# Kernel tuning notes

Measured on AMD Instinct MI355X. Metric: run time of the kernel, lower is better.

Reference implementation:

```python
import jax, jax.numpy as jnp
import numpy as np

L_MAX = 3
NR = 3


def _sh_channels(x, y, z):
    # Real spherical harmonic polynomials up to l=3, in the exact channel
    # order produced by the original stack/concat/reshape sequence:
    # [Y00, Y10(z), Y20, Y30,  (Y1_10,Y1_11, Y2_10,Y2_11, Y3_10,Y3_11),
    #  (Y2_20,Y2_21, Y3_20,Y3_21), (Y3_30,Y3_31)]
    pi = np.pi
    x2, y2, z2 = x * x, y * y, z * z
    xy, yz, zx = x * y, y * z, z * x
    x3, y3, z3 = x2 * x, y2 * y, z2 * z
    x2y, y2z, z2x = x2 * y, y2 * z, z2 * x
    x2z, xy2, yz2 = x2 * z, x * y2, y * z2
    xyz = xy * z

    Y00 = jnp.full_like(x, np.sqrt(1.0 / pi) / 2.0)
    c1 = np.sqrt(3.0 / pi) / 2.0
    Y100, Y1_10, Y1_11 = c1 * z, c1 * x, c1 * y
    c2 = np.sqrt(15.0 / pi) / 2.0
    Y200 = np.sqrt(5.0 / pi) / 4.0 * (2.0 * z2 - x2 - y2)
    Y2_10, Y2_11 = c2 * zx, c2 * yz
    Y2_20, Y2_21 = np.sqrt(15.0 / pi) / 4.0 * (x2 - y2), c2 * xy
    c31 = np.sqrt(21.0 / (2.0 * pi)) / 4.0
    Y300 = np.sqrt(7.0 / pi) / 4.0 * (2.0 * z3 - 3.0 * x2z - 3.0 * y2z)
    Y3_10 = c31 * (4.0 * z2x - x3 - xy2)
    Y3_11 = c31 * (4.0 * yz2 - x2y - y3)
    Y3_20 = np.sqrt(105.0 / pi) / 4.0 * (x2z - y2z)
    Y3_21 = np.sqrt(105.0 / pi) / 2.0 * xyz
    c33 = np.sqrt(35.0 / (2.0 * pi)) / 4.0
    Y3_30 = c33 * (x3 - 3.0 * xy2)
    Y3_31 = c33 * (3.0 * x2y - y3)

    return jnp.stack([
        Y00, Y100, Y200, Y300,
        Y1_10, Y1_11, Y2_10, Y2_11, Y3_10, Y3_11,
        Y2_20, Y2_21, Y3_20, Y3_21,
        Y3_30, Y3_31,
    ], axis=-1)  # [..., 16]


def _gaussian_shells(r, n):
    # shell centers evenly spaced in [0, 1]
    centers = jnp.arange(n, dtype=r.dtype) / float(max(n - 1, 1))
    d = r[..., None] - centers  # [..., n]
    g = jnp.exp((4.0 * np.log(0.5)) * (d * d))
    return g / jnp.sum(g, axis=-1, keepdims=True)


def setup_inputs() -> dict:
    key = jax.random.key(0)
    k1, k2, k3 = jax.random.split(key, 3)
    B, V, P = 4, 4096, 64
    patches = jax.random.normal(k1, (B, V, P, 3), dtype=jnp.float32)
    frames = jax.random.normal(k2, (B, V, 3, 3), dtype=jnp.float32)
    r = jax.random.uniform(k3, (B, V, P), dtype=jnp.float32)
    return {"patches": patches, "frames": frames, "r": r}


def reference(patches, frames, r):
    # l2_normalize with tf's eps behavior
    sq = jnp.sum(patches * patches, axis=-1, keepdims=True)
    dirs = patches / jnp.sqrt(jnp.maximum(sq, 1e-12))
    # rotate directions into local frames
    proj = jnp.einsum('bvij,bvpi->bvpj', frames, dirs)  # [B,V,P,3]
    x, y, z = proj[..., 0], proj[..., 1], proj[..., 2]
    Y = _sh_channels(x, y, z)            # [B,V,P,16]
    g = _gaussian_shells(r, NR)          # [B,V,P,NR]
    return g[..., :, None] * Y[..., None, :]  # [B,V,P,NR,16]
```

## Files before the change

kernel.cpp:

```cpp
#include <hip/hip_runtime.h>


#define TPB 256
#define PT_VALS 48
#define SM_STRIDE 49

__global__ __launch_bounds__(TPB) void sph_kernel(
    const float* __restrict__ patches,
    const float* __restrict__ frames,
    const float* __restrict__ rr,
    float* __restrict__ out,
    int n_points)
{
    __shared__ float sm[TPB * SM_STRIDE];
    const int tid = threadIdx.x;
    const int q = blockIdx.x * TPB + tid;

    if (q < n_points) {
        float d0 = patches[q * 3 + 0];
        float d1 = patches[q * 3 + 1];
        float d2 = patches[q * 3 + 2];
        float sq = d0 * d0 + d1 * d1 + d2 * d2;
        float inv = rsqrtf(fmaxf(sq, 1e-12f));
        d0 *= inv; d1 *= inv; d2 *= inv;

        const int vb = (q >> 6) * 9;
        float x = frames[vb + 0] * d0 + frames[vb + 3] * d1 + frames[vb + 6] * d2;
        float y = frames[vb + 1] * d0 + frames[vb + 4] * d1 + frames[vb + 7] * d2;
        float z = frames[vb + 2] * d0 + frames[vb + 5] * d1 + frames[vb + 8] * d2;

        float x2 = x * x, y2 = y * y, z2 = z * z;
        float xy = x * y, yz = y * z, zx = z * x;
        float Y[16];
        Y[0]  = 0.28209479177387814f;
        Y[1]  = 0.4886025119029199f * z;
        Y[2]  = 0.31539156525252005f * (2.0f * z2 - x2 - y2);
        Y[3]  = 0.3731763325901154f * (2.0f * z2 * z - 3.0f * x2 * z - 3.0f * y2 * z);
        Y[4]  = 0.4886025119029199f * x;
        Y[5]  = 0.4886025119029199f * y;
        Y[6]  = 1.0925484305920792f * zx;
        Y[7]  = 1.0925484305920792f * yz;
        Y[8]  = 0.4570457994644658f * (4.0f * z2 * x - x2 * x - x * y2);
        Y[9]  = 0.4570457994644658f * (4.0f * y * z2 - x2 * y - y2 * y);
        Y[10] = 0.5462742152960396f * (x2 - y2);
        Y[11] = 1.0925484305920792f * xy;
        Y[12] = 1.4453057213202769f * (x2 * z - y2 * z);
        Y[13] = 2.8906114426405538f * (xy * z);
        Y[14] = 0.5900435899266435f * (x2 * x - 3.0f * x * y2);
        Y[15] = 0.5900435899266435f * (3.0f * x2 * y - y2 * y);

        float rv = rr[q];
        float e0 = rv, e1 = rv - 0.5f, e2 = rv - 1.0f;
        float g0 = exp2f(-4.0f * e0 * e0);
        float g1 = exp2f(-4.0f * e1 * e1);
        float g2 = exp2f(-4.0f * e2 * e2);
        float gn = 1.0f / (g0 + g1 + g2);
        g0 *= gn; g1 *= gn; g2 *= gn;

        float* s = sm + tid * SM_STRIDE;
        #pragma unroll
        for (int c = 0; c < 16; ++c) {
            s[c]      = g0 * Y[c];
            s[16 + c] = g1 * Y[c];
            s[32 + c] = g2 * Y[c];
        }
    }
    __syncthreads();

    const size_t obase = (size_t)blockIdx.x * (TPB * PT_VALS);
    const size_t total = (size_t)n_points * PT_VALS;
    #pragma unroll
    for (int j = tid; j < TPB * PT_VALS; j += TPB) {
        size_t go = obase + (size_t)j;
        if (go < total) {
            out[go] = sm[(j / PT_VALS) * SM_STRIDE + (j % PT_VALS)];
        }
    }
}

extern "C" void kernel_launch(void* const* d_in, const int* in_sizes, int n_in,
                              void* d_out, int out_size, void* d_ws, size_t ws_size,
                              hipStream_t stream) {
    const float* patches = (const float*)d_in[0];
    const float* frames  = (const float*)d_in[1];
    const float* r       = (const float*)d_in[2];
    float* out = (float*)d_out;

    const int n_points = in_sizes[2];
    const int blocks = (n_points + TPB - 1) / TPB;
    sph_kernel<<<blocks, TPB, 0, stream>>>(patches, frames, r, out, n_points);
}
```

Before: 215.8 us.

## Stage Y and shell weights separately in LDS and emit float4 stores

Instead of writing all 48 products per point into a padded LDS row and copying them out one scalar at a time, each thread stores its 16 harmonics as four float4 rows plus three normalized shell weights. The output loop then writes float4 values, doing the g*Y multiply at store time. This cuts LDS footprint (about 50 KB down to about 20 KB), which may raise occupancy, and quadruples the width of each global store. The cost is extra multiplies and index arithmetic in the output loop.

Result: faster. 210.1 us (-2.6%).

```diff
diff --git a/kernel.cpp b/kernel.cpp
--- a/kernel.cpp
+++ b/kernel.cpp
@@ -2,17 +2,19 @@
 
 
 #define TPB 256
-#define PT_VALS 48
-#define SM_STRIDE 49
+#define YSTRIDE 257
+#define GSTRIDE 257
 
 __global__ __launch_bounds__(TPB) void sph_kernel(
     const float* __restrict__ patches,
     const float* __restrict__ frames,
     const float* __restrict__ rr,
-    float* __restrict__ out,
+    float4* __restrict__ out4,
     int n_points)
 {
-    __shared__ float sm[TPB * SM_STRIDE];
+    __shared__ float4 sY[4 * YSTRIDE];
+    __shared__ float  sG[3 * GSTRIDE];
+
     const int tid = threadIdx.x;
     const int q = blockIdx.x * TPB + tid;
 
@@ -31,49 +33,56 @@
 
         float x2 = x * x, y2 = y * y, z2 = z * z;
         float xy = x * y, yz = y * z, zx = z * x;
-        float Y[16];
-        Y[0]  = 0.28209479177387814f;
-        Y[1]  = 0.4886025119029199f * z;
-        Y[2]  = 0.31539156525252005f * (2.0f * z2 - x2 - y2);
-        Y[3]  = 0.3731763325901154f * (2.0f * z2 * z - 3.0f * x2 * z - 3.0f * y2 * z);
-        Y[4]  = 0.4886025119029199f * x;
-        Y[5]  = 0.4886025119029199f * y;
-        Y[6]  = 1.0925484305920792f * zx;
-        Y[7]  = 1.0925484305920792f * yz;
-        Y[8]  = 0.4570457994644658f * (4.0f * z2 * x - x2 * x - x * y2);
-        Y[9]  = 0.4570457994644658f * (4.0f * y * z2 - x2 * y - y2 * y);
-        Y[10] = 0.5462742152960396f * (x2 - y2);
-        Y[11] = 1.0925484305920792f * xy;
-        Y[12] = 1.4453057213202769f * (x2 * z - y2 * z);
-        Y[13] = 2.8906114426405538f * (xy * z);
-        Y[14] = 0.5900435899266435f * (x2 * x - 3.0f * x * y2);
-        Y[15] = 0.5900435899266435f * (3.0f * x2 * y - y2 * y);
+        float Y0  = 0.28209479177387814f;
+        float Y1  = 0.4886025119029199f * z;
+        float Y2  = 0.31539156525252005f * (2.0f * z2 - x2 - y2);
+        float Y3  = 0.3731763325901154f * (2.0f * z2 * z - 3.0f * x2 * z - 3.0f * y2 * z);
+        float Y4  = 0.4886025119029199f * x;
+        float Y5  = 0.4886025119029199f * y;
+        float Y6  = 1.0925484305920792f * zx;
+        float Y7  = 1.0925484305920792f * yz;
+        float Y8  = 0.4570457994644658f * (4.0f * z2 * x - x2 * x - x * y2);
+        float Y9  = 0.4570457994644658f * (4.0f * y * z2 - x2 * y - y2 * y);
+        float Y10 = 0.5462742152960396f * (x2 - y2);
+        float Y11 = 1.0925484305920792f * xy;
+        float Y12 = 1.4453057213202769f * (x2 * z - y2 * z);
+        float Y13 = 2.8906114426405538f * (xy * z);
+        float Y14 = 0.5900435899266435f * (x2 * x - 3.0f * x * y2);
+        float Y15 = 0.5900435899266435f * (3.0f * x2 * y - y2 * y);
 
         float rv = rr[q];
-        float e0 = rv, e1 = rv - 0.5f, e2 = rv - 1.0f;
-        float g0 = exp2f(-4.0f * e0 * e0);
+        float e1 = rv - 0.5f, e2 = rv - 1.0f;
+        float g0 = exp2f(-4.0f * rv * rv);
         float g1 = exp2f(-4.0f * e1 * e1);
         float g2 = exp2f(-4.0f * e2 * e2);
         float gn = 1.0f / (g0 + g1 + g2);
-        g0 *= gn; g1 *= gn; g2 *= gn;
 
-        float* s = sm + tid * SM_STRIDE;
-        #pragma unroll
-        for (int c = 0; c < 16; ++c) {
-            s[c]      = g0 * Y[c];
-            s[16 + c] = g1 * Y[c];
-            s[32 + c] = g2 * Y[c];
-        }
+        sY[0 * YSTRIDE + tid] = make_float4(Y0,  Y1,  Y2,  Y3);
+        sY[1 * YSTRIDE + tid] = make_float4(Y4,  Y5,  Y6,  Y7);
+        sY[2 * YSTRIDE + tid] = make_float4(Y8,  Y9,  Y10, Y11);
+        sY[3 * YSTRIDE + tid] = make_float4(Y12, Y13, Y14, Y15);
+        sG[0 * GSTRIDE + tid] = g0 * gn;
+        sG[1 * GSTRIDE + tid] = g1 * gn;
+        sG[2 * GSTRIDE + tid] = g2 * gn;
     }
     __syncthreads();
 
-    const size_t obase = (size_t)blockIdx.x * (TPB * PT_VALS);
-    const size_t total = (size_t)n_points * PT_VALS;
+    const size_t obase = (size_t)blockIdx.x * (TPB * 12);
+    const size_t total4 = (size_t)n_points * 12;
     #pragma unroll
-    for (int j = tid; j < TPB * PT_VALS; j += TPB) {
+    for (int k = 0; k < 12; ++k) {
+        int j = tid + k * TPB;
+        int p = j / 12;
+        int qc = j - p * 12;
+        int shell = qc >> 2;
+        int c4 = qc & 3;
         size_t go = obase + (size_t)j;
-        if (go < total) {
-            out[go] = sm[(j / PT_VALS) * SM_STRIDE + (j % PT_VALS)];
+        if (go < total4) {
+            float g = sG[shell * GSTRIDE + p];
+            float4 yv = sY[c4 * YSTRIDE + p];
+            float4 o;
+            o.x = g * yv.x; o.y = g * yv.y; o.z = g * yv.z; o.w = g * yv.w;
+            out4[go] = o;
         }
     }
 }
@@ -84,9 +93,9 @@
     const float* patches = (const float*)d_in[0];
     const float* frames  = (const float*)d_in[1];
     const float* r       = (const float*)d_in[2];
-    float* out = (float*)d_out;
+    float4* out4 = (float4*)d_out;
 
     const int n_points = in_sizes[2];
     const int blocks = (n_points + TPB - 1) / TPB;
-    sph_kernel<<<blocks, TPB, 0, stream>>>(patches, frames, r, out, n_points);
+    sph_kernel<<<blocks, TPB, 0, stream>>>(patches, frames, r, out4, n_points);
 }
```
